# Optimization experiments

Measured on AMD Instinct MI355X. Metric: run time of the kernel, lower is better.

The kernel has to match this reference:

```python
import jax, jax.numpy as jnp
import numpy as np

B, L = 16384, 200
N_USERS, N_ITEMS, N_CATS, N_DUR = 1_000_000, 100_000, 1000, 50
UD, ID, CD, DD, SD = 64, 64, 16, 8, 64
UDENSE, IDENSE = 25, 3
CONCAT = UD + ID + CD + DD + UDENSE + IDENSE + SD  # 244
NE, EH, EO, NT = 8, 256, 128, 2
T1, T2 = 64, 32  # tower dims
AH1, AH2 = 64, 16  # DIN attention hidden dims
NEG_INF = -1e9


def setup_inputs() -> dict:
    key = jax.random.key(0)
    ks = iter(jax.random.split(key, 40))
    nrm = lambda shape, s: jax.random.normal(next(ks), shape, jnp.float32) * s
    inp = {
        'user_id': jax.random.randint(next(ks), (B,), 0, N_USERS),
        'item_id': jax.random.randint(next(ks), (B,), 0, N_ITEMS),
        'item_category': jax.random.randint(next(ks), (B,), 0, N_CATS),
        'item_dur_bkt': jax.random.randint(next(ks), (B,), 0, N_DUR),
        'user_dense': jax.random.normal(next(ks), (B, UDENSE), jnp.float32),
        'item_dense': jax.random.normal(next(ks), (B, IDENSE), jnp.float32),
        'history_seq': jax.random.randint(next(ks), (B, L), 0, N_ITEMS + 1),
    }
    # embeddings (std=0.01 as in _init_weights); hist row 0 is padding_idx -> zero
    inp['user_E'] = nrm((N_USERS, UD), 0.01)
    inp['item_E'] = nrm((N_ITEMS, ID), 0.01)
    inp['cat_E'] = nrm((N_CATS, CD), 0.01)
    inp['dur_E'] = nrm((N_DUR, DD), 0.01)
    inp['hist_E'] = nrm((N_ITEMS + 1, SD), 0.01).at[0].set(0.0)
    inp['Wproj'] = nrm((ID, SD), 0.12)  # xavier-ish for target_proj (no bias)
    # DIN attention MLP: 4*SD -> 64 -> 16 -> 1
    inp['aW1'] = nrm((4 * SD, AH1), 0.06); inp['ab1'] = jnp.zeros((AH1,), jnp.float32)
    inp['aW2'] = nrm((AH1, AH2), 0.15);    inp['ab2'] = jnp.zeros((AH2,), jnp.float32)
    inp['aW3'] = nrm((AH2, 1), 0.3);       inp['ab3'] = jnp.zeros((1,), jnp.float32)
    # stacked experts: concat -> 256 -> 128 (ReLU both)
    inp['eW1'] = nrm((NE, CONCAT, EH), 0.06); inp['eb1'] = jnp.zeros((NE, EH), jnp.float32)
    inp['eW2'] = nrm((NE, EH, EO), 0.06);     inp['eb2'] = jnp.zeros((NE, EO), jnp.float32)
    # per-task gates: concat -> NE softmax
    inp['gW'] = nrm((NT, CONCAT, NE), 0.06); inp['gb'] = jnp.zeros((NT, NE), jnp.float32)
    # stacked towers: 128 -> 64 -> 32 -> 1
    inp['tW1'] = nrm((NT, EO, T1), 0.09); inp['tb1'] = jnp.zeros((NT, T1), jnp.float32)
    inp['tW2'] = nrm((NT, T1, T2), 0.12); inp['tb2'] = jnp.zeros((NT, T2), jnp.float32)
    inp['tW3'] = nrm((NT, T2, 1), 0.17);  inp['tb3'] = jnp.zeros((NT, 1), jnp.float32)
    return inp


def reference(user_id, item_id, item_category, item_dur_bkt, user_dense, item_dense,
              history_seq, user_E, item_E, cat_E, dur_E, hist_E, Wproj,
              aW1, ab1, aW2, ab2, aW3, ab3,
              eW1, eb1, eW2, eb2, gW, gb,
              tW1, tb1, tW2, tb2, tW3, tb3):
    # --- feature encoding ---
    i_emb = item_E[item_id]            # (B, ID)
    u_emb = user_E[user_id]            # (B, UD)
    c_emb = cat_E[item_category]       # (B, CD)
    d_emb = dur_E[item_dur_bkt]        # (B, DD)
    h_emb = hist_E[history_seq]        # (B, L, SD)
    tgt = (i_emb @ Wproj)[:, None, :]  # (B, 1, SD)
    t = jnp.broadcast_to(tgt, h_emb.shape)
    # DIN attention features: [target, hist, target-hist, target*hist]
    feat = jnp.concatenate([t, h_emb, t - h_emb, t * h_emb], axis=-1)  # (B, L, 4*SD)
    h = jax.nn.relu(feat @ aW1 + ab1)
    h = jax.nn.relu(h @ aW2 + ab2)
    scores = (h @ aW3 + ab3)[..., 0]   # (B, L)
    scores = jnp.where(history_seq == 0, NEG_INF, scores)
    attn = jax.nn.softmax(scores, axis=-1)
    pooled = jnp.einsum('bl,bld->bd', attn, h_emb)  # (B, SD)
    shared = jnp.concatenate([u_emb, i_emb, c_emb, d_emb, user_dense, item_dense, pooled], axis=-1)  # (B, CONCAT)
    # --- experts (batched GEMM) ---
    eh = jax.nn.relu(jnp.einsum('bc,ech->beh', shared, eW1) + eb1)
    eo = jax.nn.relu(jnp.einsum('beh,eho->beo', eh, eW2) + eb2)  # (B, NE, EO)
    # --- per-task gating + towers ---
    gate = jax.nn.softmax(jnp.einsum('bc,tce->bte', shared, gW) + gb, axis=-1)  # (B, T, NE)
    ti = jnp.einsum('bte,beo->bto', gate, eo)  # (B, T, EO)
    x = jax.nn.relu(jnp.einsum('bto,toh->bth', ti, tW1) + tb1)
    x = jax.nn.relu(jnp.einsum('bth,thk->btk', x, tW2) + tb2)
    logit = (jnp.einsum('btk,tkj->btj', x, tW3) + tb3)[..., 0]  # (B, T)
    pred = jax.nn.sigmoid(logit)
    return pred[:, 0], pred[:, 1]
```

## Files before the change

kernel.cpp:

```cpp
#include <hip/hip_runtime.h>
#include <hip/hip_bf16.h>
#include <cstdint>
#include <cmath>


typedef __attribute__((ext_vector_type(8))) short bfrag;
typedef __attribute__((ext_vector_type(4))) float f32x4;

__device__ __forceinline__ unsigned short f2bf(float f) {
  __hip_bfloat16 h = __float2bfloat16(f);
  return __builtin_bit_cast(unsigned short, h);
}
__device__ __forceinline__ float bf2f(unsigned short b) {
  union { unsigned u; float f; } v; v.u = ((unsigned)b) << 16;
  return v.f;
}
__device__ __forceinline__ float bfLo(unsigned hv) {
  union { unsigned u; float f; } v; v.u = hv << 16;
  return v.f;
}
__device__ __forceinline__ float bfHi(unsigned hv) {
  union { unsigned u; float f; } v; v.u = hv & 0xffff0000u;
  return v.f;
}

#define SWZ(row, col) ((col) ^ (((row) & 7) << 3))

static constexpr size_t WS_ATTNB = 0;
static constexpr size_t WS_AW2T  = WS_ATTNB + 16384;
static constexpr size_t WS_A13   = WS_AW2T + 2048;
static constexpr size_t WS_EW1T  = WS_A13 + 16384;
static constexpr size_t WS_EW2T  = WS_EW1T + 1048576;
static constexpr size_t WS_HISTB = WS_EW2T + 524288;
static constexpr size_t WS_TGT   = WS_HISTB + 12800256;
static constexpr size_t WS_TA    = WS_TGT + 2097152;
static constexpr size_t WS_SHP   = WS_TA + 4194304;
static constexpr size_t WS_EO    = WS_SHP + 8388608;
static constexpr size_t WS_GWB   = WS_EO + 33554432;
static constexpr size_t WS_TW1B  = WS_GWB + 8192;
static constexpr size_t WS_TW2B  = WS_TW1B + 32768;
static constexpr size_t WS_WPB   = WS_TW2B + 8192;
static constexpr size_t WS_WAB   = WS_WPB + 8192;

__launch_bounds__(256)
__global__ void k0_prep(const float* __restrict__ aW1, const float* __restrict__ aW2,
                        const float* __restrict__ eW1, const float* __restrict__ eW2,
                        const float* __restrict__ hist_E,
                        const float* __restrict__ gW, const float* __restrict__ tW1,
                        const float* __restrict__ tW2, const float* __restrict__ Wproj,
                        unsigned short* __restrict__ attnBt, unsigned short* __restrict__ aW2t,
                        unsigned short* __restrict__ eW1t, unsigned short* __restrict__ eW2t,
                        unsigned short* __restrict__ hist_b,
                        unsigned short* __restrict__ gWb, unsigned short* __restrict__ tW1b,
                        unsigned short* __restrict__ tW2b,
                        unsigned short* __restrict__ Wpb, unsigned short* __restrict__ WAb) {
  int tid = blockIdx.x * blockDim.x + threadIdx.x;
  int nth = gridDim.x * blockDim.x;
  for (int i = tid; i < 64 * 128; i += nth) {
    int n = i >> 7, k = i & 127;
    float v = (k < 64) ? (aW1[(64 + k) * 64 + n] - aW1[(128 + k) * 64 + n])
                       : aW1[(128 + k) * 64 + n];
    attnBt[i] = f2bf(v);
  }
  for (int i = tid; i < 16 * 64; i += nth) {
    int n = i >> 6, k = i & 63;
    aW2t[i] = f2bf(aW2[k * 16 + n]);
  }
  for (int i = tid; i < 64 * 64; i += nth) {
    int n = i >> 6, k = i & 63;
    Wpb[i] = f2bf(Wproj[k * 64 + n]);
  }
  for (int i = tid; i < 64 * 64; i += nth) {
    int n = i >> 6, k = i & 63;
    float s = 0.f;
    for (int j = 0; j < 64; ++j)
      s += Wproj[k * 64 + j] * (aW1[j * 64 + n] + aW1[(128 + j) * 64 + n]);
    WAb[i] = f2bf(s);
  }
  for (int i = tid; i < 8 * 256 * 256; i += nth) {
    int e = i >> 16, n = (i >> 8) & 255, k = i & 255;
    eW1t[i] = (k < 244) ? f2bf(eW1[(e * 244 + k) * 256 + n]) : (unsigned short)0;
  }
  for (int i = tid; i < 8 * 128 * 256; i += nth) {
    int e = i >> 15, n = (i >> 8) & 127, k = i & 255;
    eW2t[i] = f2bf(eW2[(e * 256 + k) * 128 + n]);
  }
  for (int i = tid; i < 16 * 256; i += nth) {
    int n = i >> 8, k = i & 255, t = n >> 3, e = n & 7;
    gWb[i] = (k < 244) ? f2bf(gW[(t * 244 + k) * 8 + e]) : (unsigned short)0;
  }
  for (int i = tid; i < 2 * 64 * 128; i += nth) {
    int t = i >> 13, n = (i >> 7) & 63, k = i & 127;
    tW1b[i] = f2bf(tW1[(t * 128 + k) * 64 + n]);
  }
  for (int i = tid; i < 2 * 32 * 64; i += nth) {
    int t = i >> 11, n = (i >> 6) & 31, k = i & 63;
    tW2b[i] = f2bf(tW2[(t * 64 + k) * 32 + n]);
  }
  for (int i = tid; i < 800008; i += nth) {
    const float* src = hist_E + (size_t)i * 8;
    float4 a = *(const float4*)src;
    float4 c = *(const float4*)(src + 4);
    uint4 q;
    q.x = (unsigned)f2bf(a.x) | ((unsigned)f2bf(a.y) << 16);
    q.y = (unsigned)f2bf(a.z) | ((unsigned)f2bf(a.w) << 16);
    q.z = (unsigned)f2bf(c.x) | ((unsigned)f2bf(c.y) << 16);
    q.w = (unsigned)f2bf(c.z) | ((unsigned)f2bf(c.w) << 16);
    *(uint4*)(hist_b + (size_t)i * 8) = q;
  }
}

__launch_bounds__(256)
__global__ void k1_tgt(const int* __restrict__ item_id, const float* __restrict__ item_E,
                       const unsigned short* __restrict__ Wpb, const unsigned short* __restrict__ WAb,
                       const float* __restrict__ ab1,
                       unsigned short* __restrict__ tgt, float* __restrict__ tA) {
  int tid = threadIdx.x, w = tid >> 6, lane = tid & 63;
  int lr = lane & 15, g = lane >> 4;
  int b0 = blockIdx.x * 64 + w * 16;
  int iid = item_id[b0 + lr];
  bfrag ia[2];
#pragma unroll
  for (int kk = 0; kk < 2; ++kk) {
    const float* src = item_E + (size_t)iid * 64 + kk * 32 + g * 8;
    float4 x = *(const float4*)src;
    float4 y = *(const float4*)(src + 4);
    bfrag r;
    r[0] = (short)f2bf(x.x); r[1] = (short)f2bf(x.y);
    r[2] = (short)f2bf(x.z); r[3] = (short)f2bf(x.w);
    r[4] = (short)f2bf(y.x); r[5] = (short)f2bf(y.y);
    r[6] = (short)f2bf(y.z); r[7] = (short)f2bf(y.w);
    ia[kk] = r;
  }
  f32x4 at[4], aa[4];
#pragma unroll
  for (int i = 0; i < 4; ++i) { at[i] = (f32x4){0,0,0,0}; aa[i] = (f32x4){0,0,0,0}; }
#pragma unroll
  for (int kk = 0; kk < 2; ++kk)
#pragma unroll
    for (int nt = 0; nt < 4; ++nt) {
      bfrag wp = *(const bfrag*)(Wpb + (nt * 16 + lr) * 64 + kk * 32 + g * 8);
      at[nt] = __builtin_amdgcn_mfma_f32_16x16x32_bf16(ia[kk], wp, at[nt], 0, 0, 0);
      bfrag wa = *(const bfrag*)(WAb + (nt * 16 + lr) * 64 + kk * 32 + g * 8);
      aa[nt] = __builtin_amdgcn_mfma_f32_16x16x32_bf16(ia[kk], wa, aa[nt], 0, 0, 0);
    }
#pragma unroll
  for (int nt = 0; nt < 4; ++nt) {
    int n = nt * 16 + lr;
    float b1 = ab1[n];
#pragma unroll
    for (int r = 0; r < 4; ++r) {
      int m = b0 + g * 4 + r;
      tgt[(size_t)m * 64 + n] = f2bf(at[nt][r]);
      tA[(size_t)m * 64 + n] = aa[nt][r] + b1;
    }
  }
}

__launch_bounds__(256)
__global__ void k3a_assemble(const int* __restrict__ user_id, const int* __restrict__ item_id,
                             const int* __restrict__ item_cat, const int* __restrict__ item_dur,
                             const float* __restrict__ user_dense, const float* __restrict__ item_dense,
                             const float* __restrict__ user_E, const float* __restrict__ item_E,
                             const float* __restrict__ cat_E, const float* __restrict__ dur_E,
                             unsigned short* __restrict__ shared_p) {
  int tid = threadIdx.x, w = tid >> 6, lane = tid & 63;
  int b = blockIdx.x * 4 + w;
  unsigned short* row = shared_p + (size_t)b * 256;
  row[lane]      = f2bf(user_E[(size_t)user_id[b] * 64 + lane]);
  row[64 + lane] = f2bf(item_E[(size_t)item_id[b] * 64 + lane]);
  if (lane < 16) row[128 + lane] = f2bf(cat_E[item_cat[b] * 16 + lane]);
  if (lane < 8)  row[144 + lane] = f2bf(dur_E[item_dur[b] * 8 + lane]);
  if (lane < 25) row[152 + lane] = f2bf(user_dense[b * 25 + lane]);
  if (lane < 3)  row[177 + lane] = f2bf(item_dense[b * 3 + lane]);
  if (lane < 12) row[244 + lane] = 0;
}

__launch_bounds__(256, 4)
__global__ void k2_attn(const int* __restrict__ hist_seq, const unsigned short* __restrict__ hist_b,
                        const unsigned short* __restrict__ tgt, const float* __restrict__ tA,
                        const unsigned short* __restrict__ attnBt_g, const unsigned short* __restrict__ aW2t_g,
                        const float* __restrict__ ab2, const float* __restrict__ aW3,
                        unsigned short* __restrict__ shared_p) {
  __shared__ unsigned short sH1[208 * 64];
  __shared__ int   ids[256];
  __shared__ float tv[64], tAv[64];
  __shared__ float sSc[256];
  __shared__ float red[8];
  int b = blockIdx.x;
  int tid = threadIdx.x, w = tid >> 6, lane = tid & 63;
  int lr = lane & 15, g = lane >> 4;

  ids[tid] = (tid < 200) ? hist_seq[(size_t)b * 200 + tid] : 0;
  if (tid < 64) tv[tid] = bf2f(tgt[(size_t)b * 64 + tid]);
  else if (tid < 128) tAv[tid - 64] = tA[(size_t)b * 64 + (tid - 64)];

  bfrag b2fr[2];
#pragma unroll
  for (int kk = 0; kk < 2; ++kk)
    b2fr[kk] = *(const bfrag*)(aW2t_g + lr * 64 + kk * 32 + g * 8);
  f32x4 ab2v4 = *(const f32x4*)(ab2 + g * 4);
  f32x4 aW3v4 = *(const f32x4*)(aW3 + g * 4);
  __syncthreads();

  {
    int n = tid >> 2, k0 = (tid & 3) * 16;
    const unsigned short* rowp = attnBt_g + n * 128;
    unsigned short a23[16], a4[16], mo[16];
    *(uint4*)(a23)     = *(const uint4*)(rowp + k0);
    *(uint4*)(a23 + 8) = *(const uint4*)(rowp + k0 + 8);
    *(uint4*)(a4)      = *(const uint4*)(rowp + 64 + k0);
    *(uint4*)(a4 + 8)  = *(const uint4*)(rowp + 64 + k0 + 8);
#pragma unroll
    for (int i = 0; i < 16; ++i)
      mo[i] = f2bf(bf2f(a23[i]) + tv[k0 + i] * bf2f(a4[i]));
    *(uint4*)(sH1 + n * 64 + SWZ(n, k0))     = *(uint4*)(mo);
    *(uint4*)(sH1 + n * 64 + SWZ(n, k0 + 8)) = *(uint4*)(mo + 8);
  }
  __syncthreads();

  bfrag mfr[4][2];
#pragma unroll
  for (int nt = 0; nt < 4; ++nt)
#pragma unroll
    for (int kk = 0; kk < 2; ++kk) {
      int n = nt * 16 + lr;
      mfr[nt][kk] = *(const bfrag*)(sH1 + n * 64 + SWZ(n, kk * 32 + g * 8));
    }
  __syncthreads();

  bfrag h0s[4], h1s[4];
#pragma unroll
  for (int s = 0; s < 4; ++s) {
    int mt = w + 4 * s;
    int m = mt * 16 + lr;
    const unsigned short* hrow = hist_b + (size_t)ids[m] * 64;
    h0s[s] = *(const bfrag*)(hrow + g * 8);
    h1s[s] = *(const bfrag*)(hrow + 32 + g * 8);
    if (mt < 13) {
      f32x4 acc[4] = {{0,0,0,0},{0,0,0,0},{0,0,0,0},{0,0,0,0}};
#pragma unroll
      for (int nt = 0; nt < 4; ++nt) {
        acc[nt] = __builtin_amdgcn_mfma_f32_16x16x32_bf16(mfr[nt][0], h0s[s], acc[nt], 0, 0, 0);
        acc[nt] = __builtin_amdgcn_mfma_f32_16x16x32_bf16(mfr[nt][1], h1s[s], acc[nt], 0, 0, 0);
      }
#pragma unroll
      for (int nt = 0; nt < 4; ++nt) {
        f32x4 ta4 = *(const f32x4*)(tAv + nt * 16 + g * 4);
        unsigned lo = (unsigned)f2bf(fmaxf(acc[nt][0] + ta4[0], 0.f))
                    | ((unsigned)f2bf(fmaxf(acc[nt][1] + ta4[1], 0.f)) << 16);
        unsigned hi = (unsigned)f2bf(fmaxf(acc[nt][2] + ta4[2], 0.f))
                    | ((unsigned)f2bf(fmaxf(acc[nt][3] + ta4[3], 0.f)) << 16);
        uint2 pk; pk.x = lo; pk.y = hi;
        *(uint2*)(sH1 + m * 64 + SWZ(m, nt * 16 + g * 4)) = pk;
      }
    }
  }
  __syncthreads();

#pragma unroll
  for (int s = 0; s < 4; ++s) {
    int mt = w + 4 * s;
    if (mt < 13) {
      int m = mt * 16 + lr;
      f32x4 acc2 = {0.f, 0.f, 0.f, 0.f};
#pragma unroll
      for (int kk = 0; kk < 2; ++kk) {
        bfrag hb = *(const bfrag*)(sH1 + m * 64 + SWZ(m, kk * 32 + g * 8));
        acc2 = __builtin_amdgcn_mfma_f32_16x16x32_bf16(b2fr[kk], hb, acc2, 0, 0, 0);
      }
      float p = 0.f;
#pragma unroll
      for (int r = 0; r < 4; ++r)
        p += fmaxf(acc2[r] + ab2v4[r], 0.f) * aW3v4[r];
      p += __shfl_xor(p, 16);
      p += __shfl_xor(p, 32);
      if (lane < 16) sSc[m] = p;
    }
  }
  __syncthreads();

  bool valid = false; float sc0 = 0.f;
  if (tid < 200 && ids[tid] != 0) { valid = true; sc0 = sSc[tid]; }
  float v = valid ? sc0 : -3.0e38f;
#pragma unroll
  for (int d = 1; d < 64; d <<= 1) v = fmaxf(v, __shfl_xor(v, d));
  if (lane == 0) red[w] = v;
  __syncthreads();
  float mx = fmaxf(fmaxf(red[0], red[1]), fmaxf(red[2], red[3]));
  float p = valid ? __expf(sc0 - mx) : 0.f;
  float s = p;
#pragma unroll
  for (int d = 1; d < 64; d <<= 1) s += __shfl_xor(s, d);
  if (lane == 0) red[4 + w] = s;
  sSc[tid] = p;
  __syncthreads();

  {
    float pacc[16];
#pragma unroll
    for (int i = 0; i < 16; ++i) pacc[i] = 0.f;
#pragma unroll
    for (int s2 = 0; s2 < 4; ++s2) {
      int m = (w + 4 * s2) * 16 + lr;
      float pm = sSc[m];
#pragma unroll
      for (int i = 0; i < 8; ++i) {
        pacc[i]     += pm * bf2f((unsigned short)h0s[s2][i]);
        pacc[8 + i] += pm * bf2f((unsigned short)h1s[s2][i]);
      }
    }
    float* sf = (float*)sH1;
#pragma unroll
    for (int i = 0; i < 16; ++i) sf[tid * 17 + i] = pacc[i];
  }
  __syncthreads();
  {
    int d = tid & 63, ww = tid >> 6;
    int gg = (d & 31) >> 3, ii = (d & 7) + ((d >> 5) << 3);
    const float* sf = (const float*)sH1;
    float part = 0.f;
#pragma unroll
    for (int l2 = 0; l2 < 16; ++l2)
      part += sf[(ww * 64 + gg * 16 + l2) * 17 + ii];
    sSc[tid] = part;
  }
  __syncthreads();
  if (tid < 64) {
    float denom = red[4] + red[5] + red[6] + red[7] + 1e-30f;
    float tot = sSc[tid] + sSc[64 + tid] + sSc[128 + tid] + sSc[192 + tid];
    shared_p[(size_t)b * 256 + 180 + tid] = f2bf(tot / denom);
  }
}

__launch_bounds__(256, 2)
__global__ void k3b_experts(const unsigned short* __restrict__ shared_p,
                            const unsigned short* __restrict__ eW1t, const unsigned short* __restrict__ eW2t,
                            const float* __restrict__ eb1, const float* __restrict__ eb2,
                            unsigned short* __restrict__ eo_ws) {
  __shared__ unsigned short sX[64 * 256];
  __shared__ unsigned short sW[256 * 64];
  int tid = threadIdx.x, w = tid >> 6, lane = tid & 63;
  int e = blockIdx.x & 7;
  int b0 = (blockIdx.x >> 3) * 64;
  int lr = lane & 15, g = lane >> 4;

  for (int j = tid; j < 2048; j += 256) {
    int r = j >> 5, ke = (j & 31) * 8;
    uint4 v = *(const uint4*)(shared_p + (size_t)(b0 + r) * 256 + ke);
    *(uint4*)(sX + r * 256 + SWZ(r, ke)) = v;
  }
  f32x4 acc[16];
#pragma unroll
  for (int i = 0; i < 16; ++i) acc[i] = (f32x4){0.f, 0.f, 0.f, 0.f};
  const unsigned short* w1 = eW1t + (size_t)e * 256 * 256;
  for (int c = 0; c < 4; ++c) {
    __syncthreads();
    for (int j = tid; j < 2048; j += 256) {
      int n = j >> 3, ke = (j & 7) * 8;
      uint4 v = *(const uint4*)(w1 + n * 256 + c * 64 + ke);
      *(uint4*)(sW + n * 64 + SWZ(n, ke)) = v;
    }
    __syncthreads();
    int m = w * 16 + lr;
#pragma unroll
    for (int kk = 0; kk < 2; ++kk) {
      int kabs = c * 64 + kk * 32 + g * 8;
      bfrag a = *(const bfrag*)(sX + m * 256 + SWZ(m, kabs));
      int kloc = kk * 32 + g * 8;
#pragma unroll
      for (int nt = 0; nt < 16; ++nt) {
        int n = nt * 16 + lr;
        bfrag bb = *(const bfrag*)(sW + n * 64 + SWZ(n, kloc));
        acc[nt] = __builtin_amdgcn_mfma_f32_16x16x32_bf16(a, bb, acc[nt], 0, 0, 0);
      }
    }
  }
  __syncthreads();
#pragma unroll
  for (int nt = 0; nt < 16; ++nt) {
    int n = nt * 16 + lr;
    float bb = eb1[e * 256 + n];
#pragma unroll
    for (int r = 0; r < 4; ++r) {
      float vv = fmaxf(acc[nt][r] + bb, 0.f);
      int mm = w * 16 + g * 4 + r;
      sX[mm * 256 + SWZ(mm, n)] = f2bf(vv);
    }
  }
  f32x4 acc2[8];
#pragma unroll
  for (int i = 0; i < 8; ++i) acc2[i] = (f32x4){0.f, 0.f, 0.f, 0.f};
  const unsigned short* w2 = eW2t + (size_t)e * 128 * 256;
  for (int c = 0; c < 4; ++c) {
    __syncthreads();
    for (int j = tid; j < 1024; j += 256) {
      int n = j >> 3, ke = (j & 7) * 8;
      uint4 v = *(const uint4*)(w2 + n * 256 + c * 64 + ke);
      *(uint4*)(sW + n * 64 + SWZ(n, ke)) = v;
    }
    __syncthreads();
    int m = w * 16 + lr;
#pragma unroll
    for (int kk = 0; kk < 2; ++kk) {
      int kabs = c * 64 + kk * 32 + g * 8;
      bfrag a = *(const bfrag*)(sX + m * 256 + SWZ(m, kabs));
      int kloc = kk * 32 + g * 8;
#pragma unroll
      for (int nt = 0; nt < 8; ++nt) {
        int n = nt * 16 + lr;
        bfrag bb = *(const bfrag*)(sW + n * 64 + SWZ(n, kloc));
        acc2[nt] = __builtin_amdgcn_mfma_f32_16x16x32_bf16(a, bb, acc2[nt], 0, 0, 0);
      }
    }
  }
#pragma unroll
  for (int nt = 0; nt < 8; ++nt) {
    int n = nt * 16 + lr;
    float bb = eb2[e * 128 + n];
#pragma unroll
    for (int r = 0; r < 4; ++r) {
      float vv = fmaxf(acc2[nt][r] + bb, 0.f);
      int mm = w * 16 + g * 4 + r;
      eo_ws[((size_t)(b0 + mm) * 8 + e) * 128 + n] = f2bf(vv);
    }
  }
}

__launch_bounds__(256, 3)
__global__ void k4_tail(const unsigned short* __restrict__ shared_p, const unsigned short* __restrict__ eo_ws,
                        const unsigned short* __restrict__ gWb, const float* __restrict__ gb,
                        const unsigned short* __restrict__ tW1b, const float* __restrict__ tb1,
                        const unsigned short* __restrict__ tW2b, const float* __restrict__ tb2,
                        const float* __restrict__ tW3, const float* __restrict__ tb3,
                        float* __restrict__ out) {
  __shared__ float sGL[32 * 17];
  __shared__ unsigned short sTi[2 * 32 * 128];
  __shared__ unsigned short sX1[2 * 32 * 64];
  int tid = threadIdx.x, w = tid >> 6, lane = tid & 63;
  int lr = lane & 15, g = lane >> 4;
  int b0 = blockIdx.x * 32;

  if (w < 2) {
    int m = b0 + w * 16 + lr;
    f32x4 acc = {0.f, 0.f, 0.f, 0.f};
#pragma unroll
    for (int kk = 0; kk < 8; ++kk) {
      bfrag a = *(const bfrag*)(shared_p + (size_t)m * 256 + kk * 32 + g * 8);
      bfrag bb = *(const bfrag*)(gWb + lr * 256 + kk * 32 + g * 8);
      acc = __builtin_amdgcn_mfma_f32_16x16x32_bf16(a, bb, acc, 0, 0, 0);
    }
    float gbv = gb[lr];
#pragma unroll
    for (int r = 0; r < 4; ++r)
      sGL[(w * 16 + g * 4 + r) * 17 + lr] = acc[r] + gbv;
  }
  __syncthreads();

  if (tid < 64) {
    int row = tid >> 1, t = tid & 1;
    float* p = sGL + row * 17 + t * 8;
    float mx = -3e38f;
#pragma unroll
    for (int e = 0; e < 8; ++e) mx = fmaxf(mx, p[e]);
    float sum = 0.f; float pe[8];
#pragma unroll
    for (int e = 0; e < 8; ++e) { pe[e] = __expf(p[e] - mx); sum += pe[e]; }
    float inv = 1.f / sum;
#pragma unroll
    for (int e = 0; e < 8; ++e) p[e] = pe[e] * inv;
  }
  __syncthreads();

  {
    int row = tid >> 3, q = tid & 7, t = q >> 2, o0 = (q & 3) * 32;
    const float* gp = sGL + row * 17 + t * 8;
    float accL[16], accH[16];
#pragma unroll
    for (int j = 0; j < 16; ++j) { accL[j] = 0.f; accH[j] = 0.f; }
    const unsigned short* base = eo_ws + ((size_t)(b0 + row) * 8) * 128 + o0;
#pragma unroll
    for (int e = 0; e < 8; ++e) {
      float ge = gp[e];
      const unsigned short* p = base + e * 128;
#pragma unroll
      for (int c = 0; c < 4; ++c) {
        uint4 v = *(const uint4*)(p + c * 8);
        const unsigned* u = (const unsigned*)&v;
#pragma unroll
        for (int j = 0; j < 4; ++j) {
          accL[c * 4 + j] += ge * bfLo(u[j]);
          accH[c * 4 + j] += ge * bfHi(u[j]);
        }
      }
    }
    unsigned short ob[32];
#pragma unroll
    for (int j = 0; j < 16; ++j) {
      ob[2 * j]     = f2bf(accL[j]);
      ob[2 * j + 1] = f2bf(accH[j]);
    }
#pragma unroll
    for (int c = 0; c < 4; ++c)
      *(uint4*)(sTi + t * 4096 + row * 128 + SWZ(row, o0 + c * 8)) = *(const uint4*)(ob + c * 8);
  }
  __syncthreads();

  int t = w >> 1, mt = w & 1;
  {
    f32x4 acc[4] = {{0.f,0.f,0.f,0.f},{0.f,0.f,0.f,0.f},{0.f,0.f,0.f,0.f},{0.f,0.f,0.f,0.f}};
    int ml = mt * 16 + lr;
#pragma unroll
    for (int kk = 0; kk < 4; ++kk) {
      bfrag a = *(const bfrag*)(sTi + t * 4096 + ml * 128 + SWZ(ml, kk * 32 + g * 8));
#pragma unroll
      for (int nt = 0; nt < 4; ++nt) {
        bfrag bb = *(const bfrag*)(tW1b + t * 8192 + (nt * 16 + lr) * 128 + kk * 32 + g * 8);
        acc[nt] = __builtin_amdgcn_mfma_f32_16x16x32_bf16(a, bb, acc[nt], 0, 0, 0);
      }
    }
#pragma unroll
    for (int nt = 0; nt < 4; ++nt) {
      int n = nt * 16 + lr;
      float bias = tb1[t * 64 + n];
#pragma unroll
      for (int r = 0; r < 4; ++r) {
        float x = fmaxf(acc[nt][r] + bias, 0.f);
        int row = mt * 16 + g * 4 + r;
        sX1[t * 2048 + row * 64 + SWZ(row, n)] = f2bf(x);
      }
    }
  }
  __syncthreads();

  {
    f32x4 acc[2] = {{0.f,0.f,0.f,0.f},{0.f,0.f,0.f,0.f}};
    int ml = mt * 16 + lr;
#pragma unroll
    for (int kk = 0; kk < 2; ++kk) {
      bfrag a = *(const bfrag*)(sX1 + t * 2048 + ml * 64 + SWZ(ml, kk * 32 + g * 8));
#pragma unroll
      for (int nt = 0; nt < 2; ++nt) {
        bfrag bb = *(const bfrag*)(tW2b + t * 2048 + (nt * 16 + lr) * 64 + kk * 32 + g * 8);
        acc[nt] = __builtin_amdgcn_mfma_f32_16x16x32_bf16(a, bb, acc[nt], 0, 0, 0);
      }
    }
    float part[4] = {0.f, 0.f, 0.f, 0.f};
#pragma unroll
    for (int nt = 0; nt < 2; ++nt) {
      int n = nt * 16 + lr;
      float bias = tb2[t * 32 + n];
      float w3 = tW3[t * 32 + n];
#pragma unroll
      for (int r = 0; r < 4; ++r)
        part[r] += fmaxf(acc[nt][r] + bias, 0.f) * w3;
    }
#pragma unroll
    for (int d = 1; d < 16; d <<= 1)
#pragma unroll
      for (int r = 0; r < 4; ++r) part[r] += __shfl_xor(part[r], d);
    if (lr == 0) {
      float b3 = tb3[t];
#pragma unroll
      for (int r = 0; r < 4; ++r) {
        float logit = part[r] + b3;
        out[(size_t)t * 16384 + b0 + mt * 16 + g * 4 + r] = 1.f / (1.f + __expf(-logit));
      }
    }
  }
}

extern "C" void kernel_launch(void* const* d_in, const int* in_sizes, int n_in,
                              void* d_out, int out_size, void* d_ws, size_t ws_size,
                              hipStream_t stream) {
  const int*   user_id    = (const int*)  d_in[0];
  const int*   item_id    = (const int*)  d_in[1];
  const int*   item_cat   = (const int*)  d_in[2];
  const int*   item_dur   = (const int*)  d_in[3];
  const float* user_dense = (const float*)d_in[4];
  const float* item_dense = (const float*)d_in[5];
  const int*   hist_seq   = (const int*)  d_in[6];
  const float* user_E     = (const float*)d_in[7];
  const float* item_E     = (const float*)d_in[8];
  const float* cat_E      = (const float*)d_in[9];
  const float* dur_E      = (const float*)d_in[10];
  const float* hist_E     = (const float*)d_in[11];
  const float* Wproj      = (const float*)d_in[12];
  const float* aW1        = (const float*)d_in[13];
  const float* ab1        = (const float*)d_in[14];
  const float* aW2        = (const float*)d_in[15];
  const float* ab2        = (const float*)d_in[16];
  const float* aW3        = (const float*)d_in[17];
  const float* eW1        = (const float*)d_in[19];
  const float* eb1        = (const float*)d_in[20];
  const float* eW2        = (const float*)d_in[21];
  const float* eb2        = (const float*)d_in[22];
  const float* gW         = (const float*)d_in[23];
  const float* gb         = (const float*)d_in[24];
  const float* tW1        = (const float*)d_in[25];
  const float* tb1        = (const float*)d_in[26];
  const float* tW2        = (const float*)d_in[27];
  const float* tb2        = (const float*)d_in[28];
  const float* tW3        = (const float*)d_in[29];
  const float* tb3        = (const float*)d_in[30];
  float* out = (float*)d_out;
  char* ws = (char*)d_ws;

  unsigned short* attnBt  = (unsigned short*)(ws + WS_ATTNB);
  unsigned short* aW2t    = (unsigned short*)(ws + WS_AW2T);
  unsigned short* eW1t    = (unsigned short*)(ws + WS_EW1T);
  unsigned short* eW2t    = (unsigned short*)(ws + WS_EW2T);
  unsigned short* hist_b  = (unsigned short*)(ws + WS_HISTB);
  unsigned short* tgt     = (unsigned short*)(ws + WS_TGT);
  float*          tA      = (float*)         (ws + WS_TA);
  unsigned short* shared_p= (unsigned short*)(ws + WS_SHP);
  unsigned short* eo_ws   = (unsigned short*)(ws + WS_EO);
  unsigned short* gWb     = (unsigned short*)(ws + WS_GWB);
  unsigned short* tW1b    = (unsigned short*)(ws + WS_TW1B);
  unsigned short* tW2b    = (unsigned short*)(ws + WS_TW2B);
  unsigned short* Wpb     = (unsigned short*)(ws + WS_WPB);
  unsigned short* WAb     = (unsigned short*)(ws + WS_WAB);

  k0_prep<<<2048, 256, 0, stream>>>(aW1, aW2, eW1, eW2, hist_E, gW, tW1, tW2, Wproj,
                                    attnBt, aW2t, eW1t, eW2t, hist_b,
                                    gWb, tW1b, tW2b, Wpb, WAb);
  k1_tgt<<<256, 256, 0, stream>>>(item_id, item_E, Wpb, WAb, ab1, tgt, tA);
  k3a_assemble<<<4096, 256, 0, stream>>>(user_id, item_id, item_cat, item_dur,
                                         user_dense, item_dense, user_E, item_E,
                                         cat_E, dur_E, shared_p);
  k2_attn<<<16384, 256, 0, stream>>>(hist_seq, hist_b, tgt, tA, attnBt, aW2t,
                                     ab2, aW3, shared_p);
  k3b_experts<<<2048, 256, 0, stream>>>(shared_p, eW1t, eW2t, eb1, eb2, eo_ws);
  k4_tail<<<512, 256, 0, stream>>>(shared_p, eo_ws, gWb, gb, tW1b, tb1, tW2b, tb2,
                                   tW3, tb3, out);
}
```

Before: 235.4 us.

## Read expert weight fragments directly from global memory instead of LDS staging

The expert MLP kernel no longer stages weight chunks into a shared-memory buffer. Each lane now loads its MFMA B fragments straight from the global weight arrays, which are shared by all blocks of the same expert and should be served mostly from cache. This drops the weight LDS buffer and the per-chunk barriers, and the occupancy hint goes from 2 to 3 blocks per CU. The cost is more global-load latency in the inner MFMA loop and less reuse of each loaded weight fragment across waves.

Measured after the change: 352.5 us. +49.7%, slower.

```diff
diff --git a/kernel.cpp b/kernel.cpp
--- a/kernel.cpp
+++ b/kernel.cpp
@@ -333,13 +333,12 @@
   }
 }
 
-__launch_bounds__(256, 2)
+__launch_bounds__(256, 3)
 __global__ void k3b_experts(const unsigned short* __restrict__ shared_p,
                             const unsigned short* __restrict__ eW1t, const unsigned short* __restrict__ eW2t,
                             const float* __restrict__ eb1, const float* __restrict__ eb2,
                             unsigned short* __restrict__ eo_ws) {
   __shared__ unsigned short sX[64 * 256];
-  __shared__ unsigned short sW[256 * 64];
   int tid = threadIdx.x, w = tid >> 6, lane = tid & 63;
   int e = blockIdx.x & 7;
   int b0 = (blockIdx.x >> 3) * 64;
@@ -350,33 +349,23 @@
     uint4 v = *(const uint4*)(shared_p + (size_t)(b0 + r) * 256 + ke);
     *(uint4*)(sX + r * 256 + SWZ(r, ke)) = v;
   }
+  __syncthreads();
+
+  int m = w * 16 + lr;
   f32x4 acc[16];
 #pragma unroll
   for (int i = 0; i < 16; ++i) acc[i] = (f32x4){0.f, 0.f, 0.f, 0.f};
   const unsigned short* w1 = eW1t + (size_t)e * 256 * 256;
-  for (int c = 0; c < 4; ++c) {
-    __syncthreads();
-    for (int j = tid; j < 2048; j += 256) {
-      int n = j >> 3, ke = (j & 7) * 8;
-      uint4 v = *(const uint4*)(w1 + n * 256 + c * 64 + ke);
-      *(uint4*)(sW + n * 64 + SWZ(n, ke)) = v;
-    }
-    __syncthreads();
-    int m = w * 16 + lr;
-#pragma unroll
-    for (int kk = 0; kk < 2; ++kk) {
-      int kabs = c * 64 + kk * 32 + g * 8;
-      bfrag a = *(const bfrag*)(sX + m * 256 + SWZ(m, kabs));
-      int kloc = kk * 32 + g * 8;
-#pragma unroll
-      for (int nt = 0; nt < 16; ++nt) {
-        int n = nt * 16 + lr;
-        bfrag bb = *(const bfrag*)(sW + n * 64 + SWZ(n, kloc));
-        acc[nt] = __builtin_amdgcn_mfma_f32_16x16x32_bf16(a, bb, acc[nt], 0, 0, 0);
-      }
-    }
-  }
-  __syncthreads();
+#pragma unroll
+  for (int kk = 0; kk < 8; ++kk) {
+    int k0 = kk * 32 + g * 8;
+    bfrag a = *(const bfrag*)(sX + m * 256 + SWZ(m, k0));
+#pragma unroll
+    for (int nt = 0; nt < 16; ++nt) {
+      bfrag bb = *(const bfrag*)(w1 + (nt * 16 + lr) * 256 + k0);
+      acc[nt] = __builtin_amdgcn_mfma_f32_16x16x32_bf16(a, bb, acc[nt], 0, 0, 0);
+    }
+  }
 #pragma unroll
   for (int nt = 0; nt < 16; ++nt) {
     int n = nt * 16 + lr;
@@ -392,26 +381,14 @@
 #pragma unroll
   for (int i = 0; i < 8; ++i) acc2[i] = (f32x4){0.f, 0.f, 0.f, 0.f};
   const unsigned short* w2 = eW2t + (size_t)e * 128 * 256;
-  for (int c = 0; c < 4; ++c) {
-    __syncthreads();
-    for (int j = tid; j < 1024; j += 256) {
-      int n = j >> 3, ke = (j & 7) * 8;
-      uint4 v = *(const uint4*)(w2 + n * 256 + c * 64 + ke);
-      *(uint4*)(sW + n * 64 + SWZ(n, ke)) = v;
-    }
-    __syncthreads();
-    int m = w * 16 + lr;
-#pragma unroll
-    for (int kk = 0; kk < 2; ++kk) {
-      int kabs = c * 64 + kk * 32 + g * 8;
-      bfrag a = *(const bfrag*)(sX + m * 256 + SWZ(m, kabs));
-      int kloc = kk * 32 + g * 8;
-#pragma unroll
-      for (int nt = 0; nt < 8; ++nt) {
-        int n = nt * 16 + lr;
-        bfrag bb = *(const bfrag*)(sW + n * 64 + SWZ(n, kloc));
-        acc2[nt] = __builtin_amdgcn_mfma_f32_16x16x32_bf16(a, bb, acc2[nt], 0, 0, 0);
-      }
+#pragma unroll
+  for (int kk = 0; kk < 8; ++kk) {
+    int k0 = kk * 32 + g * 8;
+    bfrag a = *(const bfrag*)(sX + m * 256 + SWZ(m, k0));
+#pragma unroll
+    for (int nt = 0; nt < 8; ++nt) {
+      bfrag bb = *(const bfrag*)(w2 + (nt * 16 + lr) * 256 + k0);
+      acc2[nt] = __builtin_amdgcn_mfma_f32_16x16x32_bf16(a, bb, acc2[nt], 0, 0, 0);
     }
   }
 #pragma unroll
```
